# Performance work log

Hardware: AMD Instinct MI355X
Metric: run time of the kernel (lower is better)

Reference implementation:

```python
import jax, jax.numpy as jnp
import numpy as np
import math

B, S, D, H = 2, 2048, 1024, 16
DH = D // H  # 64
K = 16       # relative-position clipping window (module hardcodes self.k = 16)


def setup_inputs() -> dict:
    key = jax.random.key(0)
    ks = jax.random.split(key, 16)
    p = lambda k, shape: (jax.random.normal(k, shape, dtype=jnp.float32) * 0.02)
    return {
        "query": jax.random.normal(ks[0], (B, S, D), dtype=jnp.float32),
        "key": jax.random.normal(ks[1], (B, S, D), dtype=jnp.float32),
        "value": jax.random.normal(ks[2], (B, S, D), dtype=jnp.float32),
        "q_mask": jnp.zeros((B, S), dtype=bool),
        "kv_mask": jnp.zeros((B, S), dtype=bool),
        "use_subseq_mask": 1,
        "Wq": p(ks[3], (D, D)), "bq": p(ks[4], (D,)),
        "Wk": p(ks[5], (D, D)), "bk": p(ks[6], (D,)),
        "Wv": p(ks[7], (D, D)), "bv": p(ks[8], (D,)),
        "Wo": p(ks[9], (D, D)), "bo": p(ks[10], (D,)),
        "wk_emb": p(ks[11], (2 * K + 1, DH)),
        "wv_emb": p(ks[12], (2 * K + 1, DH)),
    }


def _proj(x, W, b, pad_mask):
    # torch Linear: x @ W.T + b; then view(B,S,H,DH) -> (B,H,S,DH), zero padded positions
    h = jnp.einsum('bsd,ed->bse', x, W) + b
    h = h.reshape(x.shape[0], x.shape[1], H, DH).transpose(0, 2, 1, 3)
    return jnp.where(pad_mask[:, None, :, None], 0.0, h)


def reference(query, key, value, q_mask, kv_mask, use_subseq_mask,
              Wq, bq, Wk, bk, Wv, bv, Wo, bo, wk_emb, wv_emb):
    b = query.shape[0]
    q = _proj(query, Wq, bq, q_mask)   # [B,H,Sq,DH]
    k = _proj(key, Wk, bk, kv_mask)    # [B,H,Sk,DH]
    v = _proj(value, Wv, bv, kv_mask)  # [B,H,Sk,DH]
    Sq, Sk = q.shape[2], k.shape[2]

    # clipped relative positions: pos[i,j] = clip(j-i, -K, K) + K  (time_step=0)
    pos = jnp.clip(jnp.arange(Sk)[None, :] - jnp.arange(Sk)[:, None], -K, K) + K
    pos = pos[:Sq]  # [Sq,Sk]

    ak = wk_emb[pos]  # [Sq,Sk,DH]
    rel_score = jnp.einsum('bhqd,qvd->bhqv', q, ak)
    scores = (jnp.einsum('bhqd,bhvd->bhqv', q, k) + rel_score) / math.sqrt(DH)

    if use_subseq_mask:
        # replaces padding mask entirely, as in the original
        mask = jnp.triu(jnp.ones((Sq, Sk), dtype=bool), k=1 + Sk - Sq)[None, None]
    else:
        mask = kv_mask[:, None, None, :]
    attn = jax.nn.softmax(jnp.where(mask, -jnp.inf, scores), axis=-1)  # [B,H,Sq,Sk]

    av = wv_emb[pos]  # [Sq,Sk,DH]
    x = jnp.einsum('bhqv,bhvd->bhqd', attn, v) + jnp.einsum('bhqv,qvd->bhqd', attn, av)

    x = x.transpose(0, 2, 1, 3).reshape(b, Sq, D)
    out = jnp.einsum('bsd,ed->bse', x, Wo) + bo
    out = jnp.where(q_mask[:, :, None], 0.0, out)
    return out, attn
```

## Files before the change

### kernel.cpp

```cpp
#include <hip/hip_runtime.h>
#include <math.h>

#define BB  2
#define SS  2048
#define DD  1024
#define HH  16
#define DHH 64
#define RK  16
#define NR  33
#define BH  (BB*HH)
#define MT  (BB*SS)
#define NT  (SS/64)
#define NF  ((size_t)BH*SS*DHH)

typedef unsigned char u8;
typedef unsigned short u16;
typedef __attribute__((ext_vector_type(8))) short short8v;
typedef __attribute__((ext_vector_type(4))) float f32x4;

__device__ __forceinline__ float4 ld4(const float* p){ return *reinterpret_cast<const float4*>(p); }
__device__ __forceinline__ void st4(float* p, float4 v){ *reinterpret_cast<float4*>(p) = v; }

__device__ __forceinline__ u16 f2bf(float f){
    union { float f; unsigned u; } v; v.f = f;
    unsigned r = v.u + 0x7fffu + ((v.u >> 16) & 1u);
    return (u16)(r >> 16);
}
__device__ __forceinline__ float bf2f(u16 h){
    union { unsigned u; float f; } v; v.u = ((unsigned)h) << 16;
    return v.f;
}

__device__ __forceinline__ void gemm_core(
    const float* __restrict__ X, const float* __restrict__ W,
    const float* __restrict__ bias, const u8* __restrict__ rmask,
    float scale, int m0, int n0, int emode,
    float* __restrict__ outf, u16* __restrict__ out_hi, u16* __restrict__ out_lo)
{
    __shared__ short8v buf[4096];
    const int t    = threadIdx.x;
    const int lane = t & 63;
    const int w    = t >> 6;
    const int wm   = w >> 1, wn = w & 1;

    f32x4 acc[4][4];
    #pragma unroll
    for (int i=0;i<4;++i)
        #pragma unroll
        for (int j=0;j<4;++j) acc[i][j] = (f32x4){0.f,0.f,0.f,0.f};

    for (int k0 = 0; k0 < DD; k0 += 64) {
        __syncthreads();
        #pragma unroll
        for (int s = 0; s < 4; ++s) {
            const int u  = t + 256*s;
            const int ri = u >> 3, kg = u & 7;
            const int iu = (ri >> 4) & 3, llx = ri & 15;
            const int cu = kg >> 2,       lh = kg & 3;
            const int idx = (((ri >> 6)*2 + cu)*4 + iu)*64 + lh*16 + llx;
            {
                const float* gp = &X[(size_t)(m0 + ri)*DD + k0 + kg*8];
                float4 x0 = ld4(gp), x1 = ld4(gp+4);
                float xs[8] = {x0.x,x0.y,x0.z,x0.w,x1.x,x1.y,x1.z,x1.w};
                short8v h, l;
                #pragma unroll
                for (int e = 0; e < 8; ++e) {
                    u16 hu = f2bf(xs[e]);
                    h[e] = (short)hu;
                    l[e] = (short)f2bf(xs[e] - bf2f(hu));
                }
                buf[idx] = h; buf[1024 + idx] = l;
            }
            {
                const float* gp = &W[(size_t)(n0 + ri)*DD + k0 + kg*8];
                float4 x0 = ld4(gp), x1 = ld4(gp+4);
                float xs[8] = {x0.x,x0.y,x0.z,x0.w,x1.x,x1.y,x1.z,x1.w};
                short8v h, l;
                #pragma unroll
                for (int e = 0; e < 8; ++e) {
                    u16 hu = f2bf(xs[e]);
                    h[e] = (short)hu;
                    l[e] = (short)f2bf(xs[e] - bf2f(hu));
                }
                buf[2048 + idx] = h; buf[3072 + idx] = l;
            }
        }
        __syncthreads();
        #pragma unroll
        for (int c = 0; c < 2; ++c) {
            short8v ah[4], al[4], bh2[4], bl[4];
            const int ab = ((wm*2 + c)*4)*64 + lane;
            const int bb = ((wn*2 + c)*4)*64 + lane;
            #pragma unroll
            for (int i = 0; i < 4; ++i) {
                ah[i]  = buf[       ab + i*64];
                al[i]  = buf[1024 + ab + i*64];
                bh2[i] = buf[2048 + bb + i*64];
                bl[i]  = buf[3072 + bb + i*64];
            }
            #pragma unroll
            for (int i = 0; i < 4; ++i)
                #pragma unroll
                for (int j = 0; j < 4; ++j) {
                    acc[i][j] = __builtin_amdgcn_mfma_f32_16x16x32_bf16(ah[i], bh2[j], acc[i][j], 0,0,0);
                    acc[i][j] = __builtin_amdgcn_mfma_f32_16x16x32_bf16(ah[i], bl[j],  acc[i][j], 0,0,0);
                    acc[i][j] = __builtin_amdgcn_mfma_f32_16x16x32_bf16(al[i], bh2[j], acc[i][j], 0,0,0);
                }
        }
    }

    const int colb = n0 + wn*64 + (lane & 15);
    const int rowb = m0 + wm*64 + ((lane >> 4) << 2);
    #pragma unroll
    for (int j = 0; j < 4; ++j) {
        const int e  = colb + j*16;
        const float be = bias[e];
        const int hh = e >> 6, dh = e & 63;
        #pragma unroll
        for (int i = 0; i < 4; ++i) {
            #pragma unroll
            for (int r = 0; r < 4; ++r) {
                const int m = rowb + i*16 + r;
                float v = (acc[i][j][r] + be) * scale;
                if (rmask[m]) v = 0.f;
                if (emode == 0) {
                    outf[(size_t)m*DD + e] = v;
                } else {
                    u16 hb = f2bf(v);
                    u16 lb = f2bf(v - bf2f(hb));
                    const int b2 = m >> 11, s2 = m & (SS-1);
                    size_t idx = (emode == 1)
                        ? ((((size_t)b2*HH + hh)*SS + s2)*DHH + dh)
                        : ((((size_t)b2*HH + hh)*DHH + dh)*SS + s2);
                    out_hi[idx] = hb; out_lo[idx] = lb;
                }
            }
        }
    }
}

__global__ __launch_bounds__(256)
void proj_qkv_mfma(const float* __restrict__ query,
                   const float* __restrict__ key,
                   const float* __restrict__ value,
                   const float* __restrict__ Wq, const float* __restrict__ bq,
                   const float* __restrict__ Wk, const float* __restrict__ bk,
                   const float* __restrict__ Wv, const float* __restrict__ bv,
                   const u8* __restrict__ q_mask, const u8* __restrict__ kv_mask,
                   u16* __restrict__ q_hi, u16* __restrict__ q_lo,
                   u16* __restrict__ k_hi, u16* __restrict__ k_lo,
                   u16* __restrict__ vT_hi, u16* __restrict__ vT_lo)
{
    const int z = blockIdx.z;
    const float* X   = (z==0)? query : (z==1)? key : value;
    const float* W   = (z==0)? Wq    : (z==1)? Wk  : Wv;
    const float* bia = (z==0)? bq    : (z==1)? bk  : bv;
    const u8* pm     = (z==0)? q_mask : kv_mask;
    u16* hi = (z==0)? q_hi : (z==1)? k_hi : vT_hi;
    u16* lo = (z==0)? q_lo : (z==1)? k_lo : vT_lo;
    const float scale = (z==0)? 0.125f : 1.0f;
    const int emode = (z==2)? 2 : 1;
    gemm_core(X, W, bia, pm, scale, blockIdx.y*128, blockIdx.x*128, emode,
              (float*)0, hi, lo);
}

__global__ __launch_bounds__(256)
void proj_out_mfma(const float* __restrict__ xbuf,
                   const float* __restrict__ Wo, const float* __restrict__ bo,
                   const u8* __restrict__ q_mask,
                   float* __restrict__ outp)
{
    gemm_core(xbuf, Wo, bo, q_mask, 1.0f, blockIdx.y*128, blockIdx.x*128, 0,
              outp, (u16*)0, (u16*)0);
}

__global__ __launch_bounds__(256)
void attn_fused(const u16* __restrict__ q_hi, const u16* __restrict__ q_lo,
                const u16* __restrict__ k_hi, const u16* __restrict__ k_lo,
                const u16* __restrict__ vT_hi, const u16* __restrict__ vT_lo,
                const float* __restrict__ wk_emb, const float* __restrict__ wv_emb,
                const u8* __restrict__ kv_mask, const int* __restrict__ use_sub_p,
                float* __restrict__ attn, float* __restrict__ xbuf)
{
    const int qt = blockIdx.x, bh = blockIdx.y;
    const int b = bh >> 4, h = bh & 15;
    const int use_sub = *use_sub_p;
    const int t = threadIdx.x;
    const int lane = t & 63, w = t >> 6;
    const int lg = lane >> 4, ll = lane & 15;

    __shared__ __align__(16) u16 Pbuf[2][64][72];
    __shared__ float qw_s[64][36];
    __shared__ float wv_s[NR][DHH];
    __shared__ float red_s[4][64][2];
    __shared__ float mid_s[64][36];
    __shared__ float stat_s[64][2];

    const int q0 = qt*64;
    const size_t qrow0 = (size_t)bh*SS + q0;
    float* attn_base = attn + ((size_t)bh*SS + q0)*SS;

    for (int idx = t; idx < 64*8; idx += 256) {
        int r = idx >> 3, c8 = idx & 7;
        *(short8v*)&Pbuf[0][r][c8*8] = *(const short8v*)&q_hi[(qrow0 + r)*DHH + c8*8];
        *(short8v*)&Pbuf[1][r][c8*8] = *(const short8v*)&q_lo[(qrow0 + r)*DHH + c8*8];
    }
    float* wkf = &mid_s[0][0];
    for (int idx = t; idx < (NR*DHH)/4; idx += 256)
        ((float4*)wkf)[idx] = ((const float4*)wk_emb)[idx];
    for (int idx = t; idx < (NR*DHH)/4; idx += 256)
        ((float4*)&wv_s[0][0])[idx] = ((const float4*)wv_emb)[idx];
    __syncthreads();

    for (int idx = t; idx < 64*NR; idx += 256) {
        int q = idx & 63, p = idx >> 6;
        float s = 0.f;
        #pragma unroll 8
        for (int d = 0; d < DHH; ++d) {
            float qv = bf2f(Pbuf[0][q][d]) + bf2f(Pbuf[1][q][d]);
            s = fmaf(qv, wkf[p*DHH + d], s);
        }
        qw_s[q][p] = s;
    }
    short8v qa_h[4][2], qa_l[4][2];
    #pragma unroll
    for (int i = 0; i < 4; ++i)
        #pragma unroll
        for (int c = 0; c < 2; ++c) {
            qa_h[i][c] = *(short8v*)&Pbuf[0][16*i + ll][c*32 + lg*8];
            qa_l[i][c] = *(short8v*)&Pbuf[1][16*i + ll][c*32 + lg*8];
        }
    __syncthreads();

    const int vtmax = use_sub ? qt : (NT-1);
    const int vcol  = 16*w + ll;

    if (use_sub) {
        const float4 z4 = make_float4(0.f,0.f,0.f,0.f);
        const int row = t >> 2, cg = (t & 3)*16;
        for (int vt = qt+1; vt < NT; ++vt) {
            float* tb = attn_base + vt*64;
            #pragma unroll
            for (int u2 = 0; u2 < 4; ++u2)
                st4(tb + (size_t)row*SS + cg + u2*4, z4);
        }
    }

    float rm[4][4], rl[4][4];
    #pragma unroll
    for (int i=0;i<4;++i)
        #pragma unroll
        for (int r=0;r<4;++r){ rm[i][r]=-INFINITY; rl[i][r]=0.f; }

    for (int vt = 0; vt <= vtmax; ++vt) {
        const size_t vrow = (size_t)bh*SS + vt*64 + vcol;
        short8v kb_h[2], kb_l[2];
        #pragma unroll
        for (int c=0;c<2;++c){
            kb_h[c] = *(const short8v*)&k_hi[vrow*DHH + c*32 + lg*8];
            kb_l[c] = *(const short8v*)&k_lo[vrow*DHH + c*32 + lg*8];
        }
        f32x4 acc[4];
        #pragma unroll
        for (int i=0;i<4;++i) acc[i]=(f32x4){0.f,0.f,0.f,0.f};
        #pragma unroll
        for (int c=0;c<2;++c)
            #pragma unroll
            for (int i=0;i<4;++i){
                acc[i] = __builtin_amdgcn_mfma_f32_16x16x32_bf16(qa_h[i][c], kb_h[c], acc[i],0,0,0);
                acc[i] = __builtin_amdgcn_mfma_f32_16x16x32_bf16(qa_h[i][c], kb_l[c], acc[i],0,0,0);
                acc[i] = __builtin_amdgcn_mfma_f32_16x16x32_bf16(qa_l[i][c], kb_h[c], acc[i],0,0,0);
            }
        const int vglob = vt*64 + vcol;
        const bool colmask = (!use_sub) && (kv_mask[b*SS + vglob] != 0);
        #pragma unroll
        for (int i=0;i<4;++i)
            #pragma unroll
            for (int r=0;r<4;++r){
                const int qloc = 16*i + 4*lg + r;
                const int qglob = q0 + qloc;
                int d = vglob - qglob; d = d<-RK?-RK:(d>RK?RK:d);
                float s = acc[i][r] + qw_s[qloc][d+RK];
                const bool msk = use_sub ? (vglob > qglob) : colmask;
                if (msk) s = -INFINITY;
                float mn = fmaxf(rm[i][r], s);
                if (mn > -INFINITY) {
                    rl[i][r] = rl[i][r]*__expf(rm[i][r]-mn) + __expf(s-mn);
                    rm[i][r] = mn;
                }
            }
    }
    #pragma unroll
    for (int i=0;i<4;++i)
        #pragma unroll
        for (int r=0;r<4;++r){
            float m = rm[i][r], l = rl[i][r];
            #pragma unroll
            for (int off=1; off<16; off<<=1){
                float om = __shfl_xor(m, off);
                float ol = __shfl_xor(l, off);
                float mn = fmaxf(m, om);
                float e1 = (m  > -INFINITY)? __expf(m  - mn) : 0.f;
                float e2 = (om > -INFINITY)? __expf(om - mn) : 0.f;
                l = l*e1 + ol*e2; m = mn;
            }
            if (ll == 0) { const int qloc = 16*i + 4*lg + r;
                red_s[w][qloc][0] = m; red_s[w][qloc][1] = l; }
        }
    __syncthreads();
    if (t < 64) {
        float m = red_s[0][t][0], l = red_s[0][t][1];
        #pragma unroll
        for (int w2=1; w2<4; ++w2){
            float om = red_s[w2][t][0], ol = red_s[w2][t][1];
            float mn = fmaxf(m, om);
            float e1 = (m >-INFINITY)? __expf(m -mn) : 0.f;
            float e2 = (om>-INFINITY)? __expf(om-mn) : 0.f;
            l = l*e1 + ol*e2; m = mn;
        }
        stat_s[t][0] = m; stat_s[t][1] = 1.f/l;
    }
    __syncthreads();

    float pb0[4][4], pb32[4][4];
    #pragma unroll
    for (int i=0;i<4;++i)
        #pragma unroll
        for (int r=0;r<4;++r){ pb0[i][r]=0.f; pb32[i][r]=0.f; }
    f32x4 xac[4];
    #pragma unroll
    for (int i=0;i<4;++i) xac[i]=(f32x4){0.f,0.f,0.f,0.f};

    for (int vt = 0; vt <= vtmax; ++vt) {
        const size_t vrow = (size_t)bh*SS + vt*64 + vcol;
        short8v kb_h[2], kb_l[2];
        #pragma unroll
        for (int c=0;c<2;++c){
            kb_h[c] = *(const short8v*)&k_hi[vrow*DHH + c*32 + lg*8];
            kb_l[c] = *(const short8v*)&k_lo[vrow*DHH + c*32 + lg*8];
        }
        f32x4 acc[4];
        #pragma unroll
        for (int i=0;i<4;++i) acc[i]=(f32x4){0.f,0.f,0.f,0.f};
        #pragma unroll
        for (int c=0;c<2;++c)
            #pragma unroll
            for (int i=0;i<4;++i){
                acc[i] = __builtin_amdgcn_mfma_f32_16x16x32_bf16(qa_h[i][c], kb_h[c], acc[i],0,0,0);
                acc[i] = __builtin_amdgcn_mfma_f32_16x16x32_bf16(qa_h[i][c], kb_l[c], acc[i],0,0,0);
                acc[i] = __builtin_amdgcn_mfma_f32_16x16x32_bf16(qa_l[i][c], kb_h[c], acc[i],0,0,0);
            }
        const int vglob = vt*64 + vcol;
        const bool colmask = (!use_sub) && (kv_mask[b*SS + vglob] != 0);

        __syncthreads();
        #pragma unroll
        for (int i=0;i<4;++i)
            #pragma unroll
            for (int r=0;r<4;++r){
                const int qloc = 16*i + 4*lg + r;
                const int qglob = q0 + qloc;
                int d = vglob - qglob; d = d<-RK?-RK:(d>RK?RK:d);
                float s = acc[i][r] + qw_s[qloc][d+RK];
                const bool msk = use_sub ? (vglob > qglob) : colmask;
                float p = msk ? 0.f : __expf(s - stat_s[qloc][0]) * stat_s[qloc][1];
                u16 hb = f2bf(p);
                Pbuf[0][qloc][vcol] = hb;
                Pbuf[1][qloc][vcol] = f2bf(p - bf2f(hb));
                if (vglob <= qglob - RK)      pb0[i][r]  += p;
                else if (vglob >= qglob + RK) pb32[i][r] += p;
            }
        __syncthreads();

        {
            float* tb = attn_base + vt*64;
            const int row = t >> 2, cg = (t & 3)*16;
            #pragma unroll
            for (int u2=0; u2<4; ++u2){
                const int c0 = cg + u2*4;
                float4 o;
                o.x = bf2f(Pbuf[0][row][c0+0]) + bf2f(Pbuf[1][row][c0+0]);
                o.y = bf2f(Pbuf[0][row][c0+1]) + bf2f(Pbuf[1][row][c0+1]);
                o.z = bf2f(Pbuf[0][row][c0+2]) + bf2f(Pbuf[1][row][c0+2]);
                o.w = bf2f(Pbuf[0][row][c0+3]) + bf2f(Pbuf[1][row][c0+3]);
                st4(tb + (size_t)row*SS + c0, o);
            }
        }
        {
            const size_t dvrow = ((size_t)bh*DHH + 16*w + ll)*SS + (size_t)vt*64;
            short8v vb_h[2], vb_l[2];
            #pragma unroll
            for (int c=0;c<2;++c){
                vb_h[c] = *(const short8v*)&vT_hi[dvrow + c*32 + lg*8];
                vb_l[c] = *(const short8v*)&vT_lo[dvrow + c*32 + lg*8];
            }
            #pragma unroll
            for (int i=0;i<4;++i){
                #pragma unroll
                for (int c=0;c<2;++c){
                    short8v pa_h = *(short8v*)&Pbuf[0][16*i + ll][c*32 + lg*8];
                    short8v pa_l = *(short8v*)&Pbuf[1][16*i + ll][c*32 + lg*8];
                    xac[i] = __builtin_amdgcn_mfma_f32_16x16x32_bf16(pa_h, vb_h[c], xac[i],0,0,0);
                    xac[i] = __builtin_amdgcn_mfma_f32_16x16x32_bf16(pa_h, vb_l[c], xac[i],0,0,0);
                    xac[i] = __builtin_amdgcn_mfma_f32_16x16x32_bf16(pa_l, vb_h[c], xac[i],0,0,0);
                }
            }
        }
    }

    #pragma unroll
    for (int i=0;i<4;++i)
        #pragma unroll
        for (int r=0;r<4;++r){
            float a0 = pb0[i][r], a2 = pb32[i][r];
            #pragma unroll
            for (int off=1; off<16; off<<=1){
                a0 += __shfl_xor(a0, off);
                a2 += __shfl_xor(a2, off);
            }
            if (ll == 0){ const int qloc = 16*i + 4*lg + r;
                red_s[w][qloc][0] = a0; red_s[w][qloc][1] = a2; }
        }
    __threadfence_block();
    __syncthreads();
    if (t < 64) {
        mid_s[t][0]  = red_s[0][t][0]+red_s[1][t][0]+red_s[2][t][0]+red_s[3][t][0];
        mid_s[t][32] = red_s[0][t][1]+red_s[1][t][1]+red_s[2][t][1]+red_s[3][t][1];
        const int qglob = q0 + t;
        const float* rowp = attn_base + (size_t)t*SS;
        #pragma unroll 4
        for (int p=1; p<32; ++p){
            const int v = qglob - RK + p;
            mid_s[t][p] = (v >= 0 && v < SS) ? rowp[v] : 0.f;
        }
    }
    float* xs = reinterpret_cast<float*>(&Pbuf[0][0][0]);
    #pragma unroll
    for (int i=0;i<4;++i)
        #pragma unroll
        for (int r=0;r<4;++r)
            xs[(16*i + 4*lg + r)*66 + 16*w + ll] = xac[i][r];
    __syncthreads();

    {
        const int row = t >> 2, dg = (t & 3)*16;
        float av[16];
        #pragma unroll
        for (int e=0;e<16;++e) av[e] = xs[row*66 + dg + e];
        #pragma unroll 4
        for (int p=0; p<NR; ++p){
            const float mm = mid_s[row][p];
            #pragma unroll
            for (int u2=0; u2<4; ++u2){
                float4 w4 = ld4(&wv_s[p][dg + u2*4]);
                av[u2*4+0] = fmaf(mm, w4.x, av[u2*4+0]);
                av[u2*4+1] = fmaf(mm, w4.y, av[u2*4+1]);
                av[u2*4+2] = fmaf(mm, w4.z, av[u2*4+2]);
                av[u2*4+3] = fmaf(mm, w4.w, av[u2*4+3]);
            }
        }
        float* xg = xbuf + ((size_t)(b*SS + q0 + row))*DD + h*DHH + dg;
        #pragma unroll
        for (int u2=0; u2<4; ++u2)
            st4(xg + u2*4, make_float4(av[u2*4+0],av[u2*4+1],av[u2*4+2],av[u2*4+3]));
    }
}

extern "C" void kernel_launch(void* const* d_in, const int* in_sizes, int n_in,
                              void* d_out, int out_size, void* d_ws, size_t ws_size,
                              hipStream_t stream)
{
    const float* query = (const float*)d_in[0];
    const float* key_  = (const float*)d_in[1];
    const float* value = (const float*)d_in[2];
    const u8*    q_mask  = (const u8*)d_in[3];
    const u8*    kv_mask = (const u8*)d_in[4];
    const int*   use_sub = (const int*)d_in[5];
    const float* Wq = (const float*)d_in[6];  const float* bq = (const float*)d_in[7];
    const float* Wk = (const float*)d_in[8];  const float* bk = (const float*)d_in[9];
    const float* Wv = (const float*)d_in[10]; const float* bv = (const float*)d_in[11];
    const float* Wo = (const float*)d_in[12]; const float* bo = (const float*)d_in[13];
    const float* wk_emb = (const float*)d_in[14];
    const float* wv_emb = (const float*)d_in[15];

    float* outp = (float*)d_out;
    float* attn = outp + (size_t)MT*DD;

    u16* wsu   = (u16*)d_ws;
    u16* q_hi  = wsu;          u16* q_lo  = wsu + NF;
    u16* k_hi  = wsu + 2*NF;   u16* k_lo  = wsu + 3*NF;
    u16* vT_hi = wsu + 4*NF;   u16* vT_lo = wsu + 5*NF;
    float* xbuf = (float*)(wsu + 6*NF);

    proj_qkv_mfma<<<dim3(8,32,3), 256, 0, stream>>>(
        query, key_, value, Wq, bq, Wk, bk, Wv, bv, q_mask, kv_mask,
        q_hi, q_lo, k_hi, k_lo, vT_hi, vT_lo);
    attn_fused<<<dim3(NT,BH), 256, 0, stream>>>(
        q_hi, q_lo, k_hi, k_lo, vT_hi, vT_lo,
        wk_emb, wv_emb, kv_mask, use_sub, attn, xbuf);
    proj_out_mfma<<<dim3(8,32), 256, 0, stream>>>(xbuf, Wo, bo, q_mask, outp);
}
```

Measured before the change: 1.419 ms.

## Pre-split weights to bf16 hi/lo and stage GEMM tiles via direct LDS loads

Adds a kernel that converts all four weight matrices to bf16 hi/lo planes once per call, so the projection GEMMs no longer redo the split for every tile. The weight tiles (and, for the output projection, the attention output, now emitted as bf16 hi/lo in head-major layout) are loaded with global_load_lds into an XOR-swizzled LDS layout. The epilogues are staged through LDS so global stores become coalesced 16-byte writes. The attention output reuses the Q buffer, which adds a kernel launch and changes the workspace layout.

New measurement: 1.283 ms. 9.6% less time.

```diff
diff --git a/kernel.cpp b/kernel.cpp
--- a/kernel.cpp
+++ b/kernel.cpp
@@ -12,6 +12,7 @@
 #define MT  (BB*SS)
 #define NT  (SS/64)
 #define NF  ((size_t)BH*SS*DHH)
+#define WN  (DD*DD)
 
 typedef unsigned char u8;
 typedef unsigned short u16;
@@ -31,17 +32,47 @@
     return v.f;
 }
 
-__device__ __forceinline__ void gemm_core(
-    const float* __restrict__ X, const float* __restrict__ W,
+__device__ __forceinline__ void gload_lds16(const void* g, void* l){
+    __builtin_amdgcn_global_load_lds(
+        (const __attribute__((address_space(1))) void*)g,
+        (__attribute__((address_space(3))) void*)l, 16, 0, 0);
+}
+
+__global__ __launch_bounds__(256)
+void conv_w_kernel(const float* __restrict__ Wq, const float* __restrict__ Wk,
+                   const float* __restrict__ Wv, const float* __restrict__ Wo,
+                   u16* __restrict__ wpl)
+{
+    const int z = blockIdx.y;
+    const float* W = (z==0)? Wq : (z==1)? Wk : (z==2)? Wv : Wo;
+    u16* hi = wpl + (size_t)z*2*WN;
+    u16* lo = hi + WN;
+    const int idx = (blockIdx.x*256 + threadIdx.x)*4;
+    float4 x = ld4(W + idx);
+    ushort4 h, l;
+    h.x = f2bf(x.x); l.x = f2bf(x.x - bf2f(h.x));
+    h.y = f2bf(x.y); l.y = f2bf(x.y - bf2f(h.y));
+    h.z = f2bf(x.z); l.z = f2bf(x.z - bf2f(h.z));
+    h.w = f2bf(x.w); l.w = f2bf(x.w - bf2f(h.w));
+    *(ushort4*)&hi[idx] = h;
+    *(ushort4*)&lo[idx] = l;
+}
+
+template<int AMODE>
+__device__ __forceinline__ void gemm2_core(
+    const float* __restrict__ Af,
+    const u16* A_hi, const u16* A_lo,
+    const u16* __restrict__ B_hi, const u16* __restrict__ B_lo,
     const float* __restrict__ bias, const u8* __restrict__ rmask,
     float scale, int m0, int n0, int emode,
-    float* __restrict__ outf, u16* __restrict__ out_hi, u16* __restrict__ out_lo)
+    float* __restrict__ outf, u16* o_hi, u16* o_lo)
 {
     __shared__ short8v buf[4096];
     const int t    = threadIdx.x;
     const int lane = t & 63;
     const int w    = t >> 6;
     const int wm   = w >> 1, wn = w & 1;
+    const int ll   = lane & 15, lg = lane >> 4;
 
     f32x4 acc[4][4];
     #pragma unroll
@@ -52,15 +83,23 @@
     for (int k0 = 0; k0 < DD; k0 += 64) {
         __syncthreads();
         #pragma unroll
-        for (int s = 0; s < 4; ++s) {
-            const int u  = t + 256*s;
-            const int ri = u >> 3, kg = u & 7;
-            const int iu = (ri >> 4) & 3, llx = ri & 15;
-            const int cu = kg >> 2,       lh = kg & 3;
-            const int idx = (((ri >> 6)*2 + cu)*4 + iu)*64 + lh*16 + llx;
-            {
-                const float* gp = &X[(size_t)(m0 + ri)*DD + k0 + kg*8];
-                float4 x0 = ld4(gp), x1 = ld4(gp+4);
+        for (int p = 0; p < 2; ++p) {
+            const u16* src = p ? B_lo : B_hi;
+            #pragma unroll
+            for (int j = 0; j < 4; ++j) {
+                const int u = j*256 + t;
+                const int r = u >> 3, kg = (u & 7) ^ (r & 7);
+                const u16* gp = src + (size_t)(n0 + r)*DD + k0 + kg*8;
+                gload_lds16(gp, &buf[(2+p)*1024 + j*256 + w*64]);
+            }
+        }
+        if (AMODE == 0) {
+            #pragma unroll
+            for (int j = 0; j < 4; ++j) {
+                const int u = j*256 + t;
+                const int r = u >> 3, kg = u & 7;
+                const float* gp = Af + (size_t)(m0 + r)*DD + k0 + kg*8;
+                float4 x0 = ld4(gp), x1 = ld4(gp + 4);
                 float xs[8] = {x0.x,x0.y,x0.z,x0.w,x1.x,x1.y,x1.z,x1.w};
                 short8v h, l;
                 #pragma unroll
@@ -69,121 +108,194 @@
                     h[e] = (short)hu;
                     l[e] = (short)f2bf(xs[e] - bf2f(hu));
                 }
-                buf[idx] = h; buf[1024 + idx] = l;
-            }
-            {
-                const float* gp = &W[(size_t)(n0 + ri)*DD + k0 + kg*8];
-                float4 x0 = ld4(gp), x1 = ld4(gp+4);
-                float xs[8] = {x0.x,x0.y,x0.z,x0.w,x1.x,x1.y,x1.z,x1.w};
-                short8v h, l;
+                const int slot = r*8 + (kg ^ (r & 7));
+                buf[slot] = h; buf[1024 + slot] = l;
+            }
+        } else {
+            #pragma unroll
+            for (int p = 0; p < 2; ++p) {
+                const u16* src = p ? A_lo : A_hi;
                 #pragma unroll
-                for (int e = 0; e < 8; ++e) {
-                    u16 hu = f2bf(xs[e]);
-                    h[e] = (short)hu;
-                    l[e] = (short)f2bf(xs[e] - bf2f(hu));
+                for (int j = 0; j < 4; ++j) {
+                    const int u = j*256 + t;
+                    const int r = u >> 3, kg = (u & 7) ^ (r & 7);
+                    const int m = m0 + r, b2 = m >> 11, s2 = m & (SS-1);
+                    const u16* gp = src + (((size_t)b2*HH + (k0 >> 6))*SS + s2)*DHH + kg*8;
+                    gload_lds16(gp, &buf[p*1024 + j*256 + w*64]);
                 }
-                buf[2048 + idx] = h; buf[3072 + idx] = l;
             }
         }
         __syncthreads();
         #pragma unroll
         for (int c = 0; c < 2; ++c) {
-            short8v ah[4], al[4], bh2[4], bl[4];
-            const int ab = ((wm*2 + c)*4)*64 + lane;
-            const int bb = ((wn*2 + c)*4)*64 + lane;
+            short8v ah[4], al[4], bh2[4], bl2[4];
             #pragma unroll
             for (int i = 0; i < 4; ++i) {
-                ah[i]  = buf[       ab + i*64];
-                al[i]  = buf[1024 + ab + i*64];
-                bh2[i] = buf[2048 + bb + i*64];
-                bl[i]  = buf[3072 + bb + i*64];
+                const int ar = wm*64 + i*16 + ll;
+                const int as = ar*8 + ((c*4 + lg) ^ (ar & 7));
+                ah[i] = buf[as]; al[i] = buf[1024 + as];
+                const int br = wn*64 + i*16 + ll;
+                const int bs = br*8 + ((c*4 + lg) ^ (br & 7));
+                bh2[i] = buf[2048 + bs]; bl2[i] = buf[3072 + bs];
             }
             #pragma unroll
             for (int i = 0; i < 4; ++i)
                 #pragma unroll
                 for (int j = 0; j < 4; ++j) {
                     acc[i][j] = __builtin_amdgcn_mfma_f32_16x16x32_bf16(ah[i], bh2[j], acc[i][j], 0,0,0);
-                    acc[i][j] = __builtin_amdgcn_mfma_f32_16x16x32_bf16(ah[i], bl[j],  acc[i][j], 0,0,0);
+                    acc[i][j] = __builtin_amdgcn_mfma_f32_16x16x32_bf16(ah[i], bl2[j], acc[i][j], 0,0,0);
                     acc[i][j] = __builtin_amdgcn_mfma_f32_16x16x32_bf16(al[i], bh2[j], acc[i][j], 0,0,0);
                 }
         }
     }
 
-    const int colb = n0 + wn*64 + (lane & 15);
-    const int rowb = m0 + wm*64 + ((lane >> 4) << 2);
-    #pragma unroll
-    for (int j = 0; j < 4; ++j) {
-        const int e  = colb + j*16;
-        const float be = bias[e];
-        const int hh = e >> 6, dh = e & 63;
-        #pragma unroll
-        for (int i = 0; i < 4; ++i) {
-            #pragma unroll
-            for (int r = 0; r < 4; ++r) {
-                const int m = rowb + i*16 + r;
-                float v = (acc[i][j][r] + be) * scale;
-                if (rmask[m]) v = 0.f;
-                if (emode == 0) {
-                    outf[(size_t)m*DD + e] = v;
-                } else {
-                    u16 hb = f2bf(v);
-                    u16 lb = f2bf(v - bf2f(hb));
-                    const int b2 = m >> 11, s2 = m & (SS-1);
-                    size_t idx = (emode == 1)
-                        ? ((((size_t)b2*HH + hh)*SS + s2)*DHH + dh)
-                        : ((((size_t)b2*HH + hh)*DHH + dh)*SS + s2);
-                    out_hi[idx] = hb; out_lo[idx] = lb;
-                }
+    const int lg4 = lg << 2;
+    if (emode == 0) {
+        float* lb = (float*)&buf[0];
+        #pragma unroll
+        for (int h2 = 0; h2 < 2; ++h2) {
+            __syncthreads();
+            if (wm == h2) {
+                #pragma unroll
+                for (int i = 0; i < 4; ++i)
+                    #pragma unroll
+                    for (int j = 0; j < 4; ++j)
+                        #pragma unroll
+                        for (int r = 0; r < 4; ++r) {
+                            const int row = i*16 + lg4 + r;
+                            const int col = wn*64 + ll + j*16;
+                            const int m = m0 + h2*64 + row;
+                            float v = (acc[i][j][r] + bias[n0+col]) * scale;
+                            if (rmask[m]) v = 0.f;
+                            lb[row*132 + col] = v;
+                        }
+            }
+            __syncthreads();
+            const int r2 = t >> 2, qd = t & 3;
+            const int m = m0 + h2*64 + r2;
+            float* dst = outf + (size_t)m*DD + n0 + qd*32;
+            const float* src = &lb[r2*132 + qd*32];
+            #pragma unroll
+            for (int k = 0; k < 8; ++k) st4(dst + k*4, ld4(src + k*4));
+        }
+    } else if (emode == 1) {
+        u16* lh  = (u16*)&buf[0];
+        u16* lo2 = lh + 64*136;
+        #pragma unroll
+        for (int h2 = 0; h2 < 2; ++h2) {
+            __syncthreads();
+            if (wm == h2) {
+                #pragma unroll
+                for (int i = 0; i < 4; ++i)
+                    #pragma unroll
+                    for (int j = 0; j < 4; ++j)
+                        #pragma unroll
+                        for (int r = 0; r < 4; ++r) {
+                            const int row = i*16 + lg4 + r;
+                            const int col = wn*64 + ll + j*16;
+                            const int m = m0 + h2*64 + row;
+                            float v = (acc[i][j][r] + bias[n0+col]) * scale;
+                            if (rmask[m]) v = 0.f;
+                            u16 hb = f2bf(v);
+                            lh [row*136 + col] = hb;
+                            lo2[row*136 + col] = f2bf(v - bf2f(hb));
+                        }
+            }
+            __syncthreads();
+            const int r2 = t >> 2, qd = t & 3;
+            const int m = m0 + h2*64 + r2, b2 = m >> 11, s2 = m & (SS-1);
+            const int e0g = n0 + qd*32;
+            const size_t base = (((size_t)b2*HH + (e0g>>6))*SS + s2)*DHH + (e0g & 63);
+            const u16* sh_ = &lh [r2*136 + qd*32];
+            const u16* sl_ = &lo2[r2*136 + qd*32];
+            #pragma unroll
+            for (int k = 0; k < 4; ++k) {
+                *(short8v*)&o_hi[base + k*8] = *(const short8v*)&sh_[k*8];
+                *(short8v*)&o_lo[base + k*8] = *(const short8v*)&sl_[k*8];
+            }
+        }
+    } else {
+        u16* lh  = (u16*)&buf[0];
+        u16* lo2 = lh + 128*72;
+        #pragma unroll
+        for (int h2 = 0; h2 < 2; ++h2) {
+            __syncthreads();
+            if (wm == h2) {
+                #pragma unroll
+                for (int i = 0; i < 4; ++i)
+                    #pragma unroll
+                    for (int j = 0; j < 4; ++j)
+                        #pragma unroll
+                        for (int r = 0; r < 4; ++r) {
+                            const int row = i*16 + lg4 + r;
+                            const int col = wn*64 + ll + j*16;
+                            const int m = m0 + h2*64 + row;
+                            float v = (acc[i][j][r] + bias[n0+col]) * scale;
+                            if (rmask[m]) v = 0.f;
+                            u16 hb = f2bf(v);
+                            lh [col*72 + row] = hb;
+                            lo2[col*72 + row] = f2bf(v - bf2f(hb));
+                        }
+            }
+            __syncthreads();
+            const int c2 = t >> 1, mh = t & 1;
+            const int e = n0 + c2;
+            const int mb = m0 + h2*64 + mh*32, b2 = mb >> 11, s0 = mb & (SS-1);
+            const size_t base = (((size_t)b2*HH + (e>>6))*DHH + (e & 63))*SS + s0;
+            const u16* sh_ = &lh [c2*72 + mh*32];
+            const u16* sl_ = &lo2[c2*72 + mh*32];
+            #pragma unroll
+            for (int k = 0; k < 4; ++k) {
+                *(short8v*)&o_hi[base + k*8] = *(const short8v*)&sh_[k*8];
+                *(short8v*)&o_lo[base + k*8] = *(const short8v*)&sl_[k*8];
             }
         }
     }
 }
 
 __global__ __launch_bounds__(256)
-void proj_qkv_mfma(const float* __restrict__ query,
-                   const float* __restrict__ key,
-                   const float* __restrict__ value,
-                   const float* __restrict__ Wq, const float* __restrict__ bq,
-                   const float* __restrict__ Wk, const float* __restrict__ bk,
-                   const float* __restrict__ Wv, const float* __restrict__ bv,
-                   const u8* __restrict__ q_mask, const u8* __restrict__ kv_mask,
-                   u16* __restrict__ q_hi, u16* __restrict__ q_lo,
-                   u16* __restrict__ k_hi, u16* __restrict__ k_lo,
-                   u16* __restrict__ vT_hi, u16* __restrict__ vT_lo)
+void proj_in_kernel(const float* __restrict__ query, const float* __restrict__ key,
+                    const float* __restrict__ value, const u16* __restrict__ wpl,
+                    const float* __restrict__ bq, const float* __restrict__ bk,
+                    const float* __restrict__ bv,
+                    const u8* __restrict__ q_mask, const u8* __restrict__ kv_mask,
+                    u16* q_hi, u16* q_lo, u16* k_hi, u16* k_lo,
+                    u16* vT_hi, u16* vT_lo)
 {
     const int z = blockIdx.z;
-    const float* X   = (z==0)? query : (z==1)? key : value;
-    const float* W   = (z==0)? Wq    : (z==1)? Wk  : Wv;
-    const float* bia = (z==0)? bq    : (z==1)? bk  : bv;
-    const u8* pm     = (z==0)? q_mask : kv_mask;
-    u16* hi = (z==0)? q_hi : (z==1)? k_hi : vT_hi;
-    u16* lo = (z==0)? q_lo : (z==1)? k_lo : vT_lo;
-    const float scale = (z==0)? 0.125f : 1.0f;
-    const int emode = (z==2)? 2 : 1;
-    gemm_core(X, W, bia, pm, scale, blockIdx.y*128, blockIdx.x*128, emode,
-              (float*)0, hi, lo);
+    const float* X    = (z==0)? query : (z==1)? key : value;
+    const u16* B_hi   = wpl + (size_t)z*2*WN;
+    const u16* B_lo   = B_hi + WN;
+    const float* bias = (z==0)? bq : (z==1)? bk : bv;
+    const u8* pm      = (z==0)? q_mask : kv_mask;
+    u16* ohi = (z==0)? q_hi : (z==1)? k_hi : vT_hi;
+    u16* olo = (z==0)? q_lo : (z==1)? k_lo : vT_lo;
+    gemm2_core<0>(X, (const u16*)0, (const u16*)0, B_hi, B_lo, bias, pm,
+                  (z==0)? 0.125f : 1.0f, blockIdx.y*128, blockIdx.x*128,
+                  (z==2)? 2 : 1, (float*)0, ohi, olo);
 }
 
 __global__ __launch_bounds__(256)
-void proj_out_mfma(const float* __restrict__ xbuf,
-                   const float* __restrict__ Wo, const float* __restrict__ bo,
-                   const u8* __restrict__ q_mask,
-                   float* __restrict__ outp)
+void proj_out_kernel2(const u16* x_hi, const u16* x_lo, const u16* __restrict__ wpl,
+                      const float* __restrict__ bo, const u8* __restrict__ q_mask,
+                      float* __restrict__ outp)
 {
-    gemm_core(xbuf, Wo, bo, q_mask, 1.0f, blockIdx.y*128, blockIdx.x*128, 0,
-              outp, (u16*)0, (u16*)0);
+    gemm2_core<1>((const float*)0, x_hi, x_lo,
+                  wpl + (size_t)3*2*WN, wpl + (size_t)3*2*WN + WN,
+                  bo, q_mask, 1.0f, blockIdx.y*128, blockIdx.x*128, 0,
+                  outp, (u16*)0, (u16*)0);
 }
 
 __global__ __launch_bounds__(256)
-void attn_fused(const u16* __restrict__ q_hi, const u16* __restrict__ q_lo,
+void attn_fused(const u16* q_hi, const u16* q_lo,
                 const u16* __restrict__ k_hi, const u16* __restrict__ k_lo,
                 const u16* __restrict__ vT_hi, const u16* __restrict__ vT_lo,
                 const float* __restrict__ wk_emb, const float* __restrict__ wv_emb,
                 const u8* __restrict__ kv_mask, const int* __restrict__ use_sub_p,
-                float* __restrict__ attn, float* __restrict__ xbuf)
+                float* __restrict__ attn, u16* x_hi, u16* x_lo)
 {
     const int qt = blockIdx.x, bh = blockIdx.y;
-    const int b = bh >> 4, h = bh & 15;
+    const int b = bh >> 4;
     const int use_sub = *use_sub_p;
     const int t = threadIdx.x;
     const int lane = t & 63, w = t >> 6;
@@ -459,10 +571,21 @@
                 av[u2*4+3] = fmaf(mm, w4.w, av[u2*4+3]);
             }
         }
-        float* xg = xbuf + ((size_t)(b*SS + q0 + row))*DD + h*DHH + dg;
-        #pragma unroll
-        for (int u2=0; u2<4; ++u2)
-            st4(xg + u2*4, make_float4(av[u2*4+0],av[u2*4+1],av[u2*4+2],av[u2*4+3]));
+        short8v hv[2], lv[2];
+        #pragma unroll
+        for (int g=0; g<2; ++g)
+            #pragma unroll
+            for (int e=0; e<8; ++e){
+                float vv = av[g*8+e];
+                u16 hb = f2bf(vv);
+                hv[g][e] = (short)hb;
+                lv[g][e] = (short)f2bf(vv - bf2f(hb));
+            }
+        const size_t base = ((size_t)bh*SS + q0 + row)*DHH + dg;
+        *(short8v*)&x_hi[base]     = hv[0];
+        *(short8v*)&x_hi[base + 8] = hv[1];
+        *(short8v*)&x_lo[base]     = lv[0];
+        *(short8v*)&x_lo[base + 8] = lv[1];
     }
 }
 
@@ -490,13 +613,15 @@
     u16* q_hi  = wsu;          u16* q_lo  = wsu + NF;
     u16* k_hi  = wsu + 2*NF;   u16* k_lo  = wsu + 3*NF;
     u16* vT_hi = wsu + 4*NF;   u16* vT_lo = wsu + 5*NF;
-    float* xbuf = (float*)(wsu + 6*NF);
-
-    proj_qkv_mfma<<<dim3(8,32,3), 256, 0, stream>>>(
-        query, key_, value, Wq, bq, Wk, bk, Wv, bv, q_mask, kv_mask,
+    u16* wpl   = wsu + 6*NF;
+
+    conv_w_kernel<<<dim3(1024,4), 256, 0, stream>>>(Wq, Wk, Wv, Wo, wpl);
+    proj_in_kernel<<<dim3(8,32,3), 256, 0, stream>>>(
+        query, key_, value, wpl, bq, bk, bv, q_mask, kv_mask,
         q_hi, q_lo, k_hi, k_lo, vT_hi, vT_lo);
     attn_fused<<<dim3(NT,BH), 256, 0, stream>>>(
         q_hi, q_lo, k_hi, k_lo, vT_hi, vT_lo,
-        wk_emb, wv_emb, kv_mask, use_sub, attn, xbuf);
-    proj_out_mfma<<<dim3(8,32), 256, 0, stream>>>(xbuf, Wo, bo, q_mask, outp);
-}
+        wk_emb, wv_emb, kv_mask, use_sub, attn, q_hi, q_lo);
+    proj_out_kernel2<<<dim3(8,32), 256, 0, stream>>>(
+        q_hi, q_lo, wpl, bo, q_mask, outp);
+}
```
